# Kernel tuning notes

Measured on AMD Instinct MI355X. Metric: run time of the kernel, lower is better.

Reference implementation:

```python
import jax, jax.numpy as jnp
import numpy as np

N_NODES = 100000
N_EDGES = 400000
IN_CH = 1024
FEAT_CH = 128
OUT_CH = 3
NEG_SLOPE = 0.01  # F.leaky_relu default


def _glorot_uniform(key, shape):
    fan_in = shape[0]
    s = 1.0 / np.sqrt(fan_in)
    return jax.random.uniform(key, shape, jnp.float32, -s, s)


def sage_conv(x, src, dst, W_l, W_r, b, num_nodes):
    """PyG SAGEConv(aggr='mean'): lin_l(mean of incoming neighbor msgs) + lin_r(x) + b."""
    msg = x[src]  # [E, d] gather of source-node features
    summed = jax.ops.segment_sum(msg, dst, num_segments=num_nodes)  # [N, d]
    deg = jax.ops.segment_sum(jnp.ones((src.shape[0],), x.dtype), dst, num_segments=num_nodes)
    agg = summed / jnp.maximum(deg, 1.0)[:, None]  # zero-in-degree nodes stay 0
    return agg @ W_l + x @ W_r + b


def setup_inputs() -> dict:
    key = jax.random.key(0)
    ks = jax.random.split(key, 11)
    features = jax.random.normal(ks[0], (N_NODES, IN_CH), jnp.float32)
    edges = jax.random.randint(ks[1], (2, N_EDGES), 0, N_NODES, jnp.int64)
    edges2 = jax.random.randint(ks[2], (2, N_EDGES), 0, N_NODES, jnp.int64)
    edge_features = jax.random.normal(ks[3], (N_EDGES, 1), jnp.float32)
    additional_feature = jax.random.normal(ks[4], (N_NODES, 20), jnp.float32)
    return {
        "features": features,
        "edges": edges,
        "edges2": edges2,
        "edge_features": edge_features,
        "additional_feature": additional_feature,
        "W1_l": _glorot_uniform(ks[5], (IN_CH, FEAT_CH)),
        "W1_r": _glorot_uniform(ks[6], (IN_CH, FEAT_CH)),
        "b1": jnp.zeros((FEAT_CH,), jnp.float32),
        "W2_l": _glorot_uniform(ks[7], (FEAT_CH, OUT_CH)),
        "W2_r": _glorot_uniform(ks[8], (FEAT_CH, OUT_CH)),
        "b2": jnp.zeros((OUT_CH,), jnp.float32),
    }


def reference(features, edges, edges2, edge_features, additional_feature,
              W1_l, W1_r, b1, W2_l, W2_r, b2):
    # use_additional_channels=False: features used as-is; edges/edge_features unused.
    src, dst = edges2[0], edges2[1]
    x = sage_conv(features, src, dst, W1_l, W1_r, b1, N_NODES)
    x = jnp.where(x >= 0, x, NEG_SLOPE * x)  # leaky_relu
    # F.dropout with training=False is identity (eval-mode reference)
    return sage_conv(x, src, dst, W2_l, W2_r, b2, N_NODES)
```

## Files before the change

### kernel.cpp

```cpp
#include <hip/hip_runtime.h>
#include <hip/hip_bf16.h>
#include <cstdint>
#include <cstddef>

#define N_NODES 100000
#define N_EDGES 400000
#define IN_CH 1024
#define FEAT_CH 128
#define OUT_CH 3
#define NEG_SLOPE 0.01f
#define NCHUNK 196

typedef __bf16 bf16x8 __attribute__((ext_vector_type(8)));
typedef unsigned short ushort8v __attribute__((ext_vector_type(8)));
typedef float f32x4 __attribute__((ext_vector_type(4)));

__device__ __forceinline__ unsigned short f32_to_bf16_rne(float f) {
    uint32_t u = __float_as_uint(f);
    u += 0x7fffu + ((u >> 16) & 1u);
    return (unsigned short)(u >> 16);
}

typedef const __attribute__((address_space(1))) unsigned char ga_t;
typedef __attribute__((address_space(3))) unsigned char la_t;
__device__ __forceinline__ void glds16(const void* g, void* l) {
    __builtin_amdgcn_global_load_lds((ga_t*)g, (la_t*)l, 16, 0, 0);
}

__global__ void wt_kernel(const float* __restrict__ Wl, const float* __restrict__ Wr,
                          unsigned short* __restrict__ Wcat)
{
    int idx = blockIdx.x * blockDim.x + threadIdx.x;
    if (idx >= 256 * IN_CH) return;
    int n = idx >> 10;
    int k = idx & 1023;
    float v = (n < FEAT_CH) ? Wl[k * FEAT_CH + n] : Wr[k * FEAT_CH + (n - FEAT_CH)];
    Wcat[idx] = f32_to_bf16_rne(v);
}

__global__ void hist_kernel(const int* __restrict__ dst, int* __restrict__ cnt)
{
    int e = blockIdx.x * blockDim.x + threadIdx.x;
    if (e >= N_EDGES) return;
    atomicAdd(&cnt[dst[e]], 1);
}

__global__ __launch_bounds__(256) void scan_p1(const int* __restrict__ cnt,
                                               int* __restrict__ rowptr,
                                               int* __restrict__ bsum)
{
    __shared__ int sdata[256];
    const int t = threadIdx.x;
    const int c0 = blockIdx.x * 512;
    const int i0 = c0 + 2 * t;
    int v0 = (i0     < N_NODES) ? cnt[i0]     : 0;
    int v1 = (i0 + 1 < N_NODES) ? cnt[i0 + 1] : 0;
    int s = v0 + v1;
    sdata[t] = s;
    __syncthreads();
    #pragma unroll
    for (int off = 1; off < 256; off <<= 1) {
        int tmp = (t >= off) ? sdata[t - off] : 0;
        __syncthreads();
        sdata[t] += tmp;
        __syncthreads();
    }
    int ex = sdata[t] - s;
    if (i0     < N_NODES) rowptr[i0]     = ex;
    if (i0 + 1 < N_NODES) rowptr[i0 + 1] = ex + v0;
    if (t == 255) bsum[blockIdx.x] = sdata[255];
}

__global__ __launch_bounds__(256) void scan_p2(const int* __restrict__ bsum,
                                               int* __restrict__ boff)
{
    __shared__ int sdata[256];
    const int t = threadIdx.x;
    int v = (t < NCHUNK) ? bsum[t] : 0;
    sdata[t] = v;
    __syncthreads();
    #pragma unroll
    for (int off = 1; off < 256; off <<= 1) {
        int tmp = (t >= off) ? sdata[t - off] : 0;
        __syncthreads();
        sdata[t] += tmp;
        __syncthreads();
    }
    if (t < NCHUNK) boff[t] = sdata[t] - v;
}

__global__ void scan_p3(int* __restrict__ rowptr, const int* __restrict__ boff)
{
    const int c0 = blockIdx.x * 512;
    const int add = boff[blockIdx.x];
    const int t = threadIdx.x;
    int i0 = c0 + 2 * t;
    if (i0     < N_NODES) rowptr[i0]     += add;
    if (i0 + 1 < N_NODES) rowptr[i0 + 1] += add;
    if (blockIdx.x == 0 && t == 0) rowptr[N_NODES] = N_EDGES;
}

__global__ void scatter_edges(const int* __restrict__ src, const int* __restrict__ dst,
                              const int* __restrict__ rowptr, int* __restrict__ cursor,
                              int* __restrict__ sorted_src)
{
    int e = blockIdx.x * blockDim.x + threadIdx.x;
    if (e >= N_EDGES) return;
    int d = dst[e];
    int pos = rowptr[d] + atomicAdd(&cursor[d], 1);
    sorted_src[pos] = src[e];
}

__global__ __launch_bounds__(256, 2) void gemm_fused(
    const float* __restrict__ X, const unsigned short* __restrict__ Wcat,
    float* __restrict__ Yl, float* __restrict__ Yr)
{
    __shared__ unsigned short As[128 * 64];
    __shared__ unsigned short Bs[256 * 64];

    const int tid   = threadIdx.x;
    const int lane  = tid & 63;
    const int wave  = tid >> 6;
    const int waveM = wave >> 1;
    const int waveN = wave & 1;
    const int q     = lane >> 4;
    const int l16   = lane & 15;
    const int esw   = l16 & 7;
    const int row0  = blockIdx.x * 128;

    const int arow = tid >> 3;
    const int au   = tid & 7;
    const int aesw = arow & 7;

    f32x4 acc[4][8] = {};
    float4 pre[8];

    auto prefetchA = [&](int k0) {
        #pragma unroll
        for (int p = 0; p < 4; ++p) {
            const int grow = row0 + p * 32 + arow;
            const float* gp = &X[(size_t)grow * IN_CH + k0 + au * 8];
            if (grow < N_NODES) {
                pre[2 * p]     = *(const float4*)gp;
                pre[2 * p + 1] = *(const float4*)(gp + 4);
            } else {
                pre[2 * p]     = make_float4(0.f, 0.f, 0.f, 0.f);
                pre[2 * p + 1] = make_float4(0.f, 0.f, 0.f, 0.f);
            }
        }
    };

    prefetchA(0);

    for (int kt = 0; kt < IN_CH / 64; ++kt) {
        const int k0 = kt * 64;

        #pragma unroll
        for (int i = 0; i < 8; ++i) {
            const int gi = wave * 8 + i;
            const int r  = gi * 8 + (lane >> 3);
            glds16(&Wcat[(size_t)r * IN_CH + k0 + (lane & 7) * 8],
                   &Bs[gi * 8 * 64]);
        }

        #pragma unroll
        for (int p = 0; p < 4; ++p) {
            const int row = p * 32 + arow;
            const int c   = au ^ aesw;
            const float4 a = pre[2 * p], b = pre[2 * p + 1];
            ushort8v o;
            o[0] = f32_to_bf16_rne(a.x); o[1] = f32_to_bf16_rne(a.y);
            o[2] = f32_to_bf16_rne(a.z); o[3] = f32_to_bf16_rne(a.w);
            o[4] = f32_to_bf16_rne(b.x); o[5] = f32_to_bf16_rne(b.y);
            o[6] = f32_to_bf16_rne(b.z); o[7] = f32_to_bf16_rne(b.w);
            *(ushort8v*)&As[row * 64 + c * 8] = o;
        }

        if (kt + 1 < IN_CH / 64) prefetchA(k0 + 64);

        __syncthreads();

        #pragma unroll
        for (int s = 0; s < 2; ++s) {
            bf16x8 af[4], bfr[8];
            const int kc = q + 4 * s;
            #pragma unroll
            for (int mi = 0; mi < 4; ++mi) {
                const int m = waveM * 64 + mi * 16 + l16;
                af[mi] = __builtin_bit_cast(
                    bf16x8, *(const ushort8v*)&As[m * 64 + (kc ^ esw) * 8]);
            }
            #pragma unroll
            for (int ni = 0; ni < 8; ++ni) {
                const int n = waveN * 128 + ni * 16 + l16;
                bfr[ni] = __builtin_bit_cast(
                    bf16x8, *(const ushort8v*)&Bs[n * 64 + kc * 8]);
            }
            #pragma unroll
            for (int mi = 0; mi < 4; ++mi)
                #pragma unroll
                for (int ni = 0; ni < 8; ++ni)
                    acc[mi][ni] = __builtin_amdgcn_mfma_f32_16x16x32_bf16(
                        af[mi], bfr[ni], acc[mi][ni], 0, 0, 0);
        }
        __syncthreads();
    }

    float* __restrict__ Ybuf = waveN ? Yr : Yl;
    #pragma unroll
    for (int mi = 0; mi < 4; ++mi) {
        #pragma unroll
        for (int r = 0; r < 4; ++r) {
            const int grow = row0 + waveM * 64 + mi * 16 + q * 4 + r;
            if (grow < N_NODES) {
                #pragma unroll
                for (int ni = 0; ni < 8; ++ni)
                    Ybuf[(size_t)grow * FEAT_CH + ni * 16 + l16] = acc[mi][ni][r];
            }
        }
    }
}

__global__ __launch_bounds__(256) void fused_agg(
    const float* __restrict__ Yl, const float* __restrict__ Yr,
    const int* __restrict__ rowptr, const int* __restrict__ sorted_src,
    const float* __restrict__ b1,
    const float* __restrict__ W2l, const float* __restrict__ W2r,
    float* __restrict__ Zl, float* __restrict__ Zr)
{
    int gid = blockIdx.x * blockDim.x + threadIdx.x;
    int node = gid >> 6;
    if (node >= N_NODES) return;
    int lane = threadIdx.x & 63;

    int beg = rowptr[node], end = rowptr[node + 1];
    float ax = 0.f, ay = 0.f;
    for (int e = beg; e < end; ++e) {
        int s = sorted_src[e];
        float2 v = *(const float2*)&Yl[(size_t)s * FEAT_CH + lane * 2];
        ax += v.x; ay += v.y;
    }
    float invd = 1.0f / fmaxf((float)(end - beg), 1.0f);
    float2 y  = *(const float2*)&Yr[(size_t)node * FEAT_CH + lane * 2];
    float2 bb = *(const float2*)&b1[lane * 2];
    float hx = fmaf(ax, invd, y.x) + bb.x;
    float hy = fmaf(ay, invd, y.y) + bb.y;
    hx = hx >= 0.f ? hx : NEG_SLOPE * hx;
    hy = hy >= 0.f ? hy : NEG_SLOPE * hy;

    const float* wl = &W2l[lane * 2 * 3];
    const float* wr = &W2r[lane * 2 * 3];
    float z[6];
    #pragma unroll
    for (int c = 0; c < 3; ++c) {
        z[c]     = hx * wl[c] + hy * wl[3 + c];
        z[3 + c] = hx * wr[c] + hy * wr[3 + c];
    }
    #pragma unroll
    for (int off = 32; off >= 1; off >>= 1)
        #pragma unroll
        for (int c = 0; c < 6; ++c)
            z[c] += __shfl_xor(z[c], off);

    if (lane == 0) {
        Zl[node * 3 + 0] = z[0]; Zl[node * 3 + 1] = z[1]; Zl[node * 3 + 2] = z[2];
        Zr[node * 3 + 0] = z[3]; Zr[node * 3 + 1] = z[4]; Zr[node * 3 + 2] = z[5];
    }
}

__global__ void agg2_final(const float* __restrict__ Zl, const float* __restrict__ Zr,
                           const int* __restrict__ rowptr, const int* __restrict__ sorted_src,
                           const float* __restrict__ b2, float* __restrict__ out)
{
    int gid = blockIdx.x * blockDim.x + threadIdx.x;
    int node = gid >> 2;
    int c = gid & 3;
    if (node >= N_NODES || c >= OUT_CH) return;
    int beg = rowptr[node], end = rowptr[node + 1];
    float acc = 0.f;
    for (int e = beg; e < end; ++e)
        acc += Zl[sorted_src[e] * 3 + c];
    float invd = 1.0f / fmaxf((float)(end - beg), 1.0f);
    out[node * 3 + c] = fmaf(acc, invd, Zr[node * 3 + c]) + b2[c];
}

extern "C" void kernel_launch(void* const* d_in, const int* in_sizes, int n_in,
                              void* d_out, int out_size, void* d_ws, size_t ws_size,
                              hipStream_t stream)
{
    const float* X   = (const float*)d_in[0];
    const int*   e2  = (const int*)d_in[2];
    const float* W1l = (const float*)d_in[5];
    const float* W1r = (const float*)d_in[6];
    const float* b1  = (const float*)d_in[7];
    const float* W2l = (const float*)d_in[8];
    const float* W2r = (const float*)d_in[9];
    const float* b2  = (const float*)d_in[10];
    const int* src = e2;
    const int* dst = e2 + N_EDGES;

    char* ws = (char*)d_ws;
    size_t off = 0;
    auto alloc = [&](size_t bytes) -> void* {
        void* p = ws + off;
        off += (bytes + 255) & ~(size_t)255;
        return p;
    };
    const size_t NB = (size_t)N_NODES * FEAT_CH * sizeof(float);
    float* Yl = (float*)alloc(NB);
    float* Yr = (float*)alloc(NB);
    float* Zl = (float*)alloc((size_t)N_NODES * OUT_CH * sizeof(float));
    float* Zr = (float*)alloc((size_t)N_NODES * OUT_CH * sizeof(float));
    unsigned short* Wcat = (unsigned short*)alloc((size_t)256 * IN_CH * 2);
    int* cnt        = (int*)alloc((size_t)N_NODES * sizeof(int));
    int* cursor     = (int*)alloc((size_t)N_NODES * sizeof(int));
    int* rowptr     = (int*)alloc((size_t)(N_NODES + 1) * sizeof(int));
    int* bsum       = (int*)alloc((size_t)NCHUNK * sizeof(int));
    int* boff       = (int*)alloc((size_t)NCHUNK * sizeof(int));
    int* sorted_src = (int*)alloc((size_t)N_EDGES * sizeof(int));

    hipMemsetAsync(cnt,    0, (size_t)N_NODES * sizeof(int), stream);
    hipMemsetAsync(cursor, 0, (size_t)N_NODES * sizeof(int), stream);

    hist_kernel<<<(N_EDGES + 255) / 256, 256, 0, stream>>>(dst, cnt);
    scan_p1<<<NCHUNK, 256, 0, stream>>>(cnt, rowptr, bsum);
    scan_p2<<<1, 256, 0, stream>>>(bsum, boff);
    scan_p3<<<NCHUNK, 256, 0, stream>>>(rowptr, boff);
    scatter_edges<<<(N_EDGES + 255) / 256, 256, 0, stream>>>(src, dst, rowptr, cursor,
                                                             sorted_src);

    wt_kernel<<<(256 * IN_CH + 255) / 256, 256, 0, stream>>>(W1l, W1r, Wcat);
    gemm_fused<<<(N_NODES + 127) / 128, 256, 0, stream>>>(X, Wcat, Yl, Yr);

    fused_agg<<<(N_NODES * 64) / 256, 256, 0, stream>>>(Yl, Yr, rowptr, sorted_src,
                                                        b1, W2l, W2r, Zl, Zr);

    agg2_final<<<(N_NODES * 4 + 255) / 256, 256, 0, stream>>>(Zl, Zr, rowptr, sorted_src,
                                                              b2, (float*)d_out);
}
```

Measured before the change: 739.8 us.

## Drop memsets, use hardware bf16 conversion, and simplify edge scatter and final aggregation

Zeroing of the degree histogram moves into the weight-transpose kernel, which removes both hipMemsetAsync calls. The separate cursor array is replaced by a copy of rowptr that edges increment atomically. Float-to-bf16 conversion now uses native __bf16 casts instead of manual rounding. GEMM tail loads clamp the row index instead of branching. The last aggregation uses one thread per node for all three channels. Together these aim to cut launch and small-kernel overhead plus some per-element instruction cost. The trade-off is that clamped tail rows load real data whose outputs are presumably discarded, and agg2 now runs with fewer threads.

```diff
diff --git a/kernel.cpp b/kernel.cpp
--- a/kernel.cpp
+++ b/kernel.cpp
@@ -15,12 +15,6 @@
 typedef unsigned short ushort8v __attribute__((ext_vector_type(8)));
 typedef float f32x4 __attribute__((ext_vector_type(4)));
 
-__device__ __forceinline__ unsigned short f32_to_bf16_rne(float f) {
-    uint32_t u = __float_as_uint(f);
-    u += 0x7fffu + ((u >> 16) & 1u);
-    return (unsigned short)(u >> 16);
-}
-
 typedef const __attribute__((address_space(1))) unsigned char ga_t;
 typedef __attribute__((address_space(3))) unsigned char la_t;
 __device__ __forceinline__ void glds16(const void* g, void* l) {
@@ -28,14 +22,16 @@
 }
 
 __global__ void wt_kernel(const float* __restrict__ Wl, const float* __restrict__ Wr,
-                          unsigned short* __restrict__ Wcat)
+                          unsigned short* __restrict__ Wcat, int* __restrict__ cnt)
 {
     int idx = blockIdx.x * blockDim.x + threadIdx.x;
+    if (idx < N_NODES) cnt[idx] = 0;
     if (idx >= 256 * IN_CH) return;
     int n = idx >> 10;
     int k = idx & 1023;
     float v = (n < FEAT_CH) ? Wl[k * FEAT_CH + n] : Wr[k * FEAT_CH + (n - FEAT_CH)];
-    Wcat[idx] = f32_to_bf16_rne(v);
+    __bf16 h = (__bf16)v;
+    Wcat[idx] = __builtin_bit_cast(unsigned short, h);
 }
 
 __global__ void hist_kernel(const int* __restrict__ dst, int* __restrict__ cnt)
@@ -89,25 +85,31 @@
     if (t < NCHUNK) boff[t] = sdata[t] - v;
 }
 
-__global__ void scan_p3(int* __restrict__ rowptr, const int* __restrict__ boff)
+__global__ void scan_p3(int* __restrict__ rowptr, const int* __restrict__ boff,
+                        int* __restrict__ rowptr_work)
 {
     const int c0 = blockIdx.x * 512;
     const int add = boff[blockIdx.x];
     const int t = threadIdx.x;
     int i0 = c0 + 2 * t;
-    if (i0     < N_NODES) rowptr[i0]     += add;
-    if (i0 + 1 < N_NODES) rowptr[i0 + 1] += add;
+    if (i0 < N_NODES) {
+        int v = rowptr[i0] + add;
+        rowptr[i0] = v; rowptr_work[i0] = v;
+    }
+    if (i0 + 1 < N_NODES) {
+        int v = rowptr[i0 + 1] + add;
+        rowptr[i0 + 1] = v; rowptr_work[i0 + 1] = v;
+    }
     if (blockIdx.x == 0 && t == 0) rowptr[N_NODES] = N_EDGES;
 }
 
 __global__ void scatter_edges(const int* __restrict__ src, const int* __restrict__ dst,
-                              const int* __restrict__ rowptr, int* __restrict__ cursor,
+                              int* __restrict__ rowptr_work,
                               int* __restrict__ sorted_src)
 {
     int e = blockIdx.x * blockDim.x + threadIdx.x;
     if (e >= N_EDGES) return;
-    int d = dst[e];
-    int pos = rowptr[d] + atomicAdd(&cursor[d], 1);
+    int pos = atomicAdd(&rowptr_work[dst[e]], 1);
     sorted_src[pos] = src[e];
 }
 
@@ -138,15 +140,11 @@
     auto prefetchA = [&](int k0) {
         #pragma unroll
         for (int p = 0; p < 4; ++p) {
-            const int grow = row0 + p * 32 + arow;
+            int grow = row0 + p * 32 + arow;
+            grow = grow < N_NODES ? grow : (N_NODES - 1);
             const float* gp = &X[(size_t)grow * IN_CH + k0 + au * 8];
-            if (grow < N_NODES) {
-                pre[2 * p]     = *(const float4*)gp;
-                pre[2 * p + 1] = *(const float4*)(gp + 4);
-            } else {
-                pre[2 * p]     = make_float4(0.f, 0.f, 0.f, 0.f);
-                pre[2 * p + 1] = make_float4(0.f, 0.f, 0.f, 0.f);
-            }
+            pre[2 * p]     = *(const float4*)gp;
+            pre[2 * p + 1] = *(const float4*)(gp + 4);
         }
     };
 
@@ -168,12 +166,12 @@
             const int row = p * 32 + arow;
             const int c   = au ^ aesw;
             const float4 a = pre[2 * p], b = pre[2 * p + 1];
-            ushort8v o;
-            o[0] = f32_to_bf16_rne(a.x); o[1] = f32_to_bf16_rne(a.y);
-            o[2] = f32_to_bf16_rne(a.z); o[3] = f32_to_bf16_rne(a.w);
-            o[4] = f32_to_bf16_rne(b.x); o[5] = f32_to_bf16_rne(b.y);
-            o[6] = f32_to_bf16_rne(b.z); o[7] = f32_to_bf16_rne(b.w);
-            *(ushort8v*)&As[row * 64 + c * 8] = o;
+            bf16x8 o;
+            o[0] = (__bf16)a.x; o[1] = (__bf16)a.y;
+            o[2] = (__bf16)a.z; o[3] = (__bf16)a.w;
+            o[4] = (__bf16)b.x; o[5] = (__bf16)b.y;
+            o[6] = (__bf16)b.z; o[7] = (__bf16)b.w;
+            *(bf16x8*)&As[row * 64 + c * 8] = o;
         }
 
         if (kt + 1 < IN_CH / 64) prefetchA(k0 + 64);
@@ -272,16 +270,18 @@
                            const int* __restrict__ rowptr, const int* __restrict__ sorted_src,
                            const float* __restrict__ b2, float* __restrict__ out)
 {
-    int gid = blockIdx.x * blockDim.x + threadIdx.x;
-    int node = gid >> 2;
-    int c = gid & 3;
-    if (node >= N_NODES || c >= OUT_CH) return;
+    int node = blockIdx.x * blockDim.x + threadIdx.x;
+    if (node >= N_NODES) return;
     int beg = rowptr[node], end = rowptr[node + 1];
-    float acc = 0.f;
-    for (int e = beg; e < end; ++e)
-        acc += Zl[sorted_src[e] * 3 + c];
+    float a0 = 0.f, a1 = 0.f, a2 = 0.f;
+    for (int e = beg; e < end; ++e) {
+        const float* zp = &Zl[sorted_src[e] * 3];
+        a0 += zp[0]; a1 += zp[1]; a2 += zp[2];
+    }
     float invd = 1.0f / fmaxf((float)(end - beg), 1.0f);
-    out[node * 3 + c] = fmaf(acc, invd, Zr[node * 3 + c]) + b2[c];
+    out[node * 3 + 0] = fmaf(a0, invd, Zr[node * 3 + 0]) + b2[0];
+    out[node * 3 + 1] = fmaf(a1, invd, Zr[node * 3 + 1]) + b2[1];
+    out[node * 3 + 2] = fmaf(a2, invd, Zr[node * 3 + 2]) + b2[2];
 }
 
 extern "C" void kernel_launch(void* const* d_in, const int* in_sizes, int n_in,
@@ -312,29 +312,27 @@
     float* Zl = (float*)alloc((size_t)N_NODES * OUT_CH * sizeof(float));
     float* Zr = (float*)alloc((size_t)N_NODES * OUT_CH * sizeof(float));
     unsigned short* Wcat = (unsigned short*)alloc((size_t)256 * IN_CH * 2);
-    int* cnt        = (int*)alloc((size_t)N_NODES * sizeof(int));
-    int* cursor     = (int*)alloc((size_t)N_NODES * sizeof(int));
-    int* rowptr     = (int*)alloc((size_t)(N_NODES + 1) * sizeof(int));
-    int* bsum       = (int*)alloc((size_t)NCHUNK * sizeof(int));
-    int* boff       = (int*)alloc((size_t)NCHUNK * sizeof(int));
-    int* sorted_src = (int*)alloc((size_t)N_EDGES * sizeof(int));
-
-    hipMemsetAsync(cnt,    0, (size_t)N_NODES * sizeof(int), stream);
-    hipMemsetAsync(cursor, 0, (size_t)N_NODES * sizeof(int), stream);
+    int* cnt         = (int*)alloc((size_t)N_NODES * sizeof(int));
+    int* rowptr      = (int*)alloc((size_t)(N_NODES + 1) * sizeof(int));
+    int* rowptr_work = (int*)alloc((size_t)N_NODES * sizeof(int));
+    int* bsum        = (int*)alloc((size_t)NCHUNK * sizeof(int));
+    int* boff        = (int*)alloc((size_t)NCHUNK * sizeof(int));
+    int* sorted_src  = (int*)alloc((size_t)N_EDGES * sizeof(int));
+
+    wt_kernel<<<(256 * IN_CH + 255) / 256, 256, 0, stream>>>(W1l, W1r, Wcat, cnt);
 
     hist_kernel<<<(N_EDGES + 255) / 256, 256, 0, stream>>>(dst, cnt);
     scan_p1<<<NCHUNK, 256, 0, stream>>>(cnt, rowptr, bsum);
     scan_p2<<<1, 256, 0, stream>>>(bsum, boff);
-    scan_p3<<<NCHUNK, 256, 0, stream>>>(rowptr, boff);
-    scatter_edges<<<(N_EDGES + 255) / 256, 256, 0, stream>>>(src, dst, rowptr, cursor,
+    scan_p3<<<NCHUNK, 256, 0, stream>>>(rowptr, boff, rowptr_work);
+    scatter_edges<<<(N_EDGES + 255) / 256, 256, 0, stream>>>(src, dst, rowptr_work,
                                                              sorted_src);
 
-    wt_kernel<<<(256 * IN_CH + 255) / 256, 256, 0, stream>>>(W1l, W1r, Wcat);
     gemm_fused<<<(N_NODES + 127) / 128, 256, 0, stream>>>(X, Wcat, Yl, Yr);
 
     fused_agg<<<(N_NODES * 64) / 256, 256, 0, stream>>>(Yl, Yr, rowptr, sorted_src,
                                                         b1, W2l, W2r, Zl, Zr);
 
-    agg2_final<<<(N_NODES * 4 + 255) / 256, 256, 0, stream>>>(Zl, Zr, rowptr, sorted_src,
-                                                              b2, (float*)d_out);
-}
+    agg2_final<<<(N_NODES + 255) / 256, 256, 0, stream>>>(Zl, Zr, rowptr, sorted_src,
+                                                          b2, (float*)d_out);
+}
```

Result: no change. 737.2 us (-0.4%).
